# Kernel tuning notes

Hardware: AMD Instinct MI355X
Metric: run time of the kernel (lower is better)

The kernel has to match this reference:

```python
import jax, jax.numpy as jnp
import numpy as np

# Module hyperparameters (BNMorph.__init__ defaults + KITTI resolution)
B, H, W = 8, 320, 1024
SEARCH_W = 7      # serachWidth
SEARCH_H = 3      # searchHeight
SPARSITY_RAD = 2
SENSE_R = 20
PIX_DW = 24.0     # pixel_distance_weight
ALPHA_DW = 0.7    # alpha_distance_weight
PIX_MUL_DW = 1.9  # pixel_mulline_distance_weight
ALPHA_PAD = 1.6   # alpha_padding
EDGE_DENSITY = 0.02


def _make_offsets():
    # Exactly mirrors BNMorph.__init__ buffer construction.
    rs = np.arange(-SEARCH_W, SEARCH_W + 1)
    cs = np.arange(-SEARCH_H, SEARCH_H + 1)
    xx, yy = np.meshgrid(rs, cs)
    xx = xx.flatten(); yy = yy.flatten()
    idx = np.argsort(xx ** 2 + yy ** 2)
    xx = xx[idx]; yy = yy[idx]
    ss = np.arange(-SPARSITY_RAD, SPARSITY_RAD + 1)
    sxx, syy = np.meshgrid(ss, ss)
    sxx = sxx.flatten(); syy = syy.flatten()
    cspan = np.arange(-SENSE_R, SENSE_R + 1)
    cxx, cyy = np.meshgrid(cspan, cspan)
    cxx = cxx.flatten(); cyy = cyy.flatten()
    ci = np.argsort(cxx ** 2 + cyy ** 2)
    cxx = cxx[ci]; cyy = cyy[ci]
    f32 = lambda a: jnp.asarray(a, dtype=jnp.float32)
    return f32(xx), f32(yy), f32(sxx), f32(syy), f32(cxx), f32(cyy)


def setup_inputs() -> dict:
    key = jax.random.key(0)
    k1, k2 = jax.random.split(key)
    binMapsrc = (jax.random.uniform(k1, (B, 1, H, W)) < EDGE_DENSITY).astype(jnp.float32)
    binMapdst = (jax.random.uniform(k2, (B, 1, H, W)) < EDGE_DENSITY).astype(jnp.float32)
    xx, yy, sxx, syy, cxx, cyy = _make_offsets()
    return {"binMapsrc": binMapsrc, "binMapdst": binMapdst,
            "xx": xx, "yy": yy, "sxx": sxx, "syy": syy, "cxx": cxx, "cyy": cyy}


def _forward(binMapsrc, binMapdst, xx, yy, sxx, syy, cxx, cyy):
    src = binMapsrc[:, 0] > 0.5  # [B,H,W] bool
    dst = binMapdst[:, 0] > 0.5
    b, h, w = src.shape

    # ---- 1. sparsity filtering of src edge points ----
    # keep an active pixel iff no active pixel precedes it (raster order)
    # inside the sparsity window -> approximates greedy sparsification.
    sdx = sxx.astype(jnp.int32); sdy = syy.astype(jnp.int32)
    prec = ((sdy < 0) | ((sdy == 0) & (sdx < 0))).astype(jnp.float32)
    Ps = jnp.pad(src.astype(jnp.float32),
                 ((0, 0), (SPARSITY_RAD, SPARSITY_RAD), (SPARSITY_RAD, SPARSITY_RAD)))

    def sp_step(acc, off):
        dx, dy, wk = off
        sl = jax.lax.dynamic_slice(Ps, (0, SPARSITY_RAD + dy, SPARSITY_RAD + dx), (b, h, w))
        return acc + sl * wk, None

    acc, _ = jax.lax.scan(sp_step, jnp.zeros((b, h, w), jnp.float32), (sdx, sdy, prec))
    kept = src & (acc < 0.5)

    # ---- 2. windowed nearest-correspondence search in dst ----
    # offsets (xx,yy) are pre-sorted by distance, so the first hit is nearest.
    qdx = xx.astype(jnp.int32); qdy = yy.astype(jnp.int32)
    Pd = jnp.pad(dst, ((0, 0), (SEARCH_H, SEARCH_H), (SEARCH_W, SEARCH_W)))

    def m_step(carry, off):
        found, vx, vy = carry
        dx, dy, dxf, dyf = off
        sl = jax.lax.dynamic_slice(Pd, (0, SEARCH_H + dy, SEARCH_W + dx), (b, h, w))
        hit = sl & kept & (~found)
        vx = jnp.where(hit, dxf, vx)
        vy = jnp.where(hit, dyf, vy)
        return (found | hit, vx, vy), None

    init = (jnp.zeros((b, h, w), bool),
            jnp.zeros((b, h, w), jnp.float32),
            jnp.zeros((b, h, w), jnp.float32))
    (found, vx, vy), _ = jax.lax.scan(m_step, init, (qdx, qdy, xx, yy))

    # ---- 3. distance-weighted morph field (splat = depthwise conv) ----
    d = jnp.sqrt(cxx ** 2 + cyy ** 2)
    wts = ALPHA_DW * jnp.exp(-d * PIX_MUL_DW / PIX_DW)
    R = SENSE_R
    K = jnp.zeros((2 * R + 1, 2 * R + 1), jnp.float32)
    K = K.at[cyy.astype(jnp.int32) + R, cxx.astype(jnp.int32) + R].set(wts)

    m = found.astype(jnp.float32)
    inp = jnp.stack([m, m * vx, m * vy], axis=1)        # [B,3,H,W]
    ker = jnp.tile(K[None, None], (3, 1, 1, 1))          # [3,1,41,41]
    out = jax.lax.conv_general_dilated(
        inp, ker, (1, 1), ((R, R), (R, R)),
        dimension_numbers=("NCHW", "OIHW", "NCHW"), feature_group_count=3)
    den = out[:, 0] + ALPHA_PAD
    dispx = out[:, 1] / den
    dispy = out[:, 2] / den

    ygrid, xgrid = jnp.meshgrid(jnp.arange(h, dtype=jnp.float32),
                                jnp.arange(w, dtype=jnp.float32), indexing="ij")
    morphedx = xgrid + dispx
    morphedy = ygrid + dispy
    orgpts_x = xgrid * m
    orgpts_y = ygrid * m
    correspts_x = (xgrid + vx) * m
    correspts_y = (ygrid + vy) * m
    return morphedx, morphedy, orgpts_x, orgpts_y, correspts_x, correspts_y


def reference(binMapsrc, binMapdst, xx, yy, sxx, syy, cxx, cyy):
    return _forward(binMapsrc, binMapdst, xx, yy, sxx, syy, cxx, cyy)
```

## Files before the change

### kernel.cpp

```cpp
#include <hip/hip_runtime.h>


#define BB 8
#define HH 320
#define WW 1024
#define N_PIX (BB*HH*WW)
#define WPI (HH*(WW/32))
#define RR 20
#define TLW 64
#define TLH 32
#define TXN (WW/TLW)
#define TYN (HH/TLH)
#define TPB (TXN*TYN)
#define N_TILES (BB*TPB)
#define NQ 105
#define CAP_MAX 512
#define PACK_OFF 16384
#define WTABN (4*42*48)
#define WTAB_OFF (PACK_OFF + 2*BB*WPI*4)
#define LISTS_OFF (WTAB_OFF + WTABN*4)

typedef unsigned long long u64;
typedef float v2f __attribute__((ext_vector_type(2)));

__global__ __launch_bounds__(256) void pack_zero(
    const float* __restrict__ src, const float* __restrict__ dst,
    unsigned* __restrict__ packed, int* __restrict__ cnt,
    float* __restrict__ wtab_g)
{
    int t = threadIdx.x;
    int i = blockIdx.x * 256 + t;
    if (i < N_TILES) cnt[i] = 0;
    if (i < WTABN) {
        int rot = i / (42 * 48);
        int rem = i - rot * (42 * 48);
        int row = rem / 48, c = rem - row * 48;
        int pc = c + rot;
        float v = 0.0f;
        if (row <= 40 && pc >= 4 && pc <= 44) {
            int dxv = pc - 24, dyv = row - 20;
            float d = sqrtf((float)(dxv * dxv + dyv * dyv));
            v = 0.7f * expf((-d * 1.9f) / 24.0f);
        }
        wtab_g[i] = v;
    }
    const float4* p = (i < (N_PIX >> 2)) ? (const float4*)src + i
                                         : (const float4*)dst + (i - (N_PIX >> 2));
    float4 v = *p;
    unsigned nib = (v.x > 0.5f ? 1u : 0u) | (v.y > 0.5f ? 2u : 0u)
                 | (v.z > 0.5f ? 4u : 0u) | (v.w > 0.5f ? 8u : 0u);
    unsigned val = nib << ((t & 7) * 4);
    val |= __shfl_xor(val, 1);
    val |= __shfl_xor(val, 2);
    val |= __shfl_xor(val, 4);
    if ((t & 7) == 0) packed[i >> 3] = val;
}

__global__ __launch_bounds__(256) void build_points(
    const unsigned* __restrict__ packed,
    const float* __restrict__ xx, const float* __restrict__ yy,
    float* __restrict__ out, int* __restrict__ cnt,
    unsigned* __restrict__ lists, int cap)
{
    __shared__ unsigned sS[6][32];
    __shared__ unsigned sD[10][32];
    __shared__ unsigned sMask[4][32];
    __shared__ unsigned sVB[4][256];
    __shared__ unsigned sPtXY[256];
    __shared__ unsigned sPk[256];
    __shared__ unsigned sPairs[1024];
    __shared__ int prank[NQ], sdxv[NQ], sdyv[NQ];
    __shared__ int lcnt[2];

    int t  = threadIdx.x;
    int y0 = blockIdx.x * 4;
    int b  = blockIdx.y;
    const unsigned* psrc = packed + (size_t)b * WPI;
    const unsigned* pdst = packed + (size_t)(BB + b) * WPI;

    if (t < 192) {
        int r = t >> 5, w = t & 31;
        int y2 = y0 - 2 + r;
        sS[r][w] = (y2 >= 0 && y2 < HH) ? psrc[(y2 << 5) + w] : 0u;
    }
    for (int i = t; i < 320; i += 256) {
        int r = i >> 5, w = i & 31;
        int y2 = y0 - 3 + r;
        sD[r][w] = (y2 >= 0 && y2 < HH) ? pdst[(y2 << 5) + w] : 0u;
    }
    if (t < NQ) {
        int dx = (int)xx[t], dy = (int)yy[t];
        sdxv[t] = dx; sdyv[t] = dy;
        prank[(dy + 3) * 15 + (dx + 7)] = t;
    }
    if (t < 2) lcnt[t] = 0;
    #pragma unroll
    for (int g = 0; g < 4; ++g) sVB[g][t] = 0;
    __syncthreads();

    if (t < 128) {
        int r = t >> 5, w = t & 31;
        unsigned C = sS[r + 2][w];
        unsigned kept = 0;
        if (C) {
            #define EXT5(row) ( (u64)((w ? (row)[w-1] : 0u) >> 30) \
                              | ((u64)(row)[w] << 2) \
                              | ((u64)((w < 31 ? (row)[w+1] : 0u) & 3u) << 34) )
            u64 a = EXT5(sS[r]) | EXT5(sS[r + 1]);
            u64 or5 = a | (a >> 1) | (a >> 2) | (a >> 3) | (a >> 4);
            u64 e2 = EXT5(sS[r + 2]);
            u64 or2 = e2 | (e2 >> 1);
            kept = C & ~(unsigned)(or5 | or2);
        }
        unsigned found = 0;
        if (kept) {
            u64 dil = 0;
            #pragma unroll
            for (int rr = 0; rr < 7; ++rr) {
                const unsigned* row = sD[r + rr];
                unsigned L = w ? row[w-1] : 0u;
                unsigned R = (w < 31) ? row[w+1] : 0u;
                dil |= (u64)(L >> 25) | ((u64)row[w] << 7) | ((u64)(R & 0x7Fu) << 39);
            }
            u64 a2 = dil | (dil >> 1);
            u64 b2 = a2 | (a2 >> 2);
            u64 c2 = b2 | (b2 >> 4);
            u64 o15 = c2 | (c2 >> 7);
            found = kept & (unsigned)o15;
        }
        sMask[r][w] = found;
        int nf = __popc(found);
        if (nf) {
            int base = atomicAdd(&lcnt[0], nf);
            unsigned fi = found;
            while (fi) {
                int bit = __builtin_ctz(fi); fi &= fi - 1;
                if (base < 256) sPtXY[base] = (unsigned)((r << 10) | (w << 5) | bit);
                ++base;
            }
        }
    }
    __syncthreads();
    int nPts = lcnt[0]; if (nPts > 256) nPts = 256;

    for (int i = t; i < nPts; i += 256) {
        unsigned e = sPtXY[i];
        int r = e >> 10, x = (int)(e & 1023u);
        int y = y0 + r;
        int x7 = x - 7;
        int j = x7 >> 5;
        int sh = x7 & 31;
        u64 lo = 0, hi = 0;
        #pragma unroll
        for (int rr = 0; rr < 7; ++rr) {
            const unsigned* row = sD[r + rr];
            unsigned W0 = (j >= 0) ? row[j] : 0u;
            unsigned W1 = (j + 1 < 32) ? row[j + 1] : 0u;
            u64 win = (((u64)W0 | ((u64)W1 << 32)) >> sh) & 0x7FFFull;
            if (rr < 4) lo |= win << (15 * rr);
            else        hi |= win << (15 * (rr - 4));
        }
        int minr = NQ - 1;
        while (lo) { int bb2 = __builtin_ctzll(lo); lo &= lo - 1; int rk = prank[bb2];      if (rk < minr) minr = rk; }
        while (hi) { int bb2 = __builtin_ctzll(hi); hi &= hi - 1; int rk = prank[60 + bb2]; if (rk < minr) minr = rk; }
        int vx = sdxv[minr], vy = sdyv[minr];

        ((unsigned char*)sVB)[(r << 10) + x] =
            (unsigned char)((vx + 7) | ((vy + 3) << 4));
        sPk[i] = (unsigned)x | ((unsigned)y << 10)
               | ((unsigned)(vx + 7) << 19) | ((unsigned)(vy + 3) << 23);

        int txl = x - RR; txl = (txl < 0 ? 0 : txl) >> 6;
        int txh = x + RR; txh = (txh > WW - 1 ? WW - 1 : txh) >> 6;
        int tyl = y - RR; tyl = (tyl < 0 ? 0 : tyl) >> 5;
        int tyh = y + RR; tyh = (tyh > HH - 1 ? HH - 1 : tyh) >> 5;
        int np = (txh - txl + 1) * (tyh - tyl + 1);
        int base = atomicAdd(&lcnt[1], np);
        for (int ty = tyl; ty <= tyh; ++ty)
            for (int tx = txl; tx <= txh; ++tx) {
                if (base < 1024)
                    sPairs[base] = ((unsigned)i << 16) | (unsigned)(b * TPB + ty * TXN + tx);
                ++base;
            }
    }
    __syncthreads();
    int nPairs = lcnt[1]; if (nPairs > 1024) nPairs = 1024;

    for (int jj = t; jj < nPairs; jj += 256) {
        unsigned pr = sPairs[jj];
        int tile = (int)(pr & 0xFFFFu);
        int i    = (int)(pr >> 16);
        int pos = atomicAdd(&cnt[tile], 1);
        if (pos < cap) lists[(size_t)tile * cap + pos] = sPk[i];
    }

    int xs = t << 2;
    int wq = t >> 3;
    int bo = xs & 31;
    size_t bbase = (size_t)b * HH * WW;
    #pragma unroll
    for (int g = 0; g < 4; ++g) {
        unsigned mw = sMask[g][wq];
        unsigned vb = sVB[g][t];
        float fy = (float)(y0 + g);
        float4 o2, o3, o4, o5;
        float* po2 = &o2.x; float* po3 = &o3.x; float* po4 = &o4.x; float* po5 = &o5.x;
        #pragma unroll
        for (int jj = 0; jj < 4; ++jj) {
            float fm = (float)((mw >> (bo + jj)) & 1u);
            unsigned by = (vb >> (8 * jj)) & 255u;
            float fvx = (float)((int)(by & 15u) - 7);
            float fvy = (float)((int)(by >> 4) - 3);
            float fx = (float)(xs + jj);
            po2[jj] = fx * fm;
            po3[jj] = fy * fm;
            po4[jj] = (fx + fvx) * fm;
            po5[jj] = (fy + fvy) * fm;
        }
        size_t idx = bbase + (size_t)(y0 + g) * WW + xs;
        *reinterpret_cast<float4*>(out + 2 * (size_t)N_PIX + idx) = o2;
        *reinterpret_cast<float4*>(out + 3 * (size_t)N_PIX + idx) = o3;
        *reinterpret_cast<float4*>(out + 4 * (size_t)N_PIX + idx) = o4;
        *reinterpret_cast<float4*>(out + 5 * (size_t)N_PIX + idx) = o5;
    }
}

__global__ __launch_bounds__(256, 4) void splat_finalize(
    const int* __restrict__ cnt, const unsigned* __restrict__ lists,
    const float* __restrict__ wtab_g,
    float* __restrict__ out, int cap)
{
    __shared__ __align__(16) float wtab[WTABN];
    __shared__ __align__(16) unsigned pts[CAP_MAX];
    int t = threadIdx.x;

    const float4* wg = (const float4*)wtab_g;
    #pragma unroll
    for (int i = 0; i < WTABN / 1024; ++i)
        ((float4*)wtab)[i * 256 + t] = wg[i * 256 + t];
    if (t < (WTABN / 4) % 256)
        ((float4*)wtab)[(WTABN / 1024) * 256 + t] = wg[(WTABN / 1024) * 256 + t];

    int txT = blockIdx.x, tyT = blockIdx.y, b = blockIdx.z;
    int tile = b * TPB + tyT * TXN + txT;
    int n = cnt[tile]; if (n > cap) n = cap;
    int n4 = (n + 3) & ~3;
    for (int i = t; i < n4; i += 256)
        pts[i] = (i < n) ? lists[(size_t)tile * cap + i] : 0xFFFFFFFFu;
    __syncthreads();

    int x0  = txT * TLW + (t & 15) * 4;
    int y0t = tyT * TLH + (t >> 4) * 2;
    int wy0 = tyT * TLH + __builtin_amdgcn_readfirstlane(t >> 6) * 8;

    v2f a0p[2][2] = {};
    v2f av[2][4]  = {};

    for (int p = 0; p < n4; p += 4) {
        uint4 P = *(const uint4*)&pts[p];
        #pragma unroll
        for (int k = 0; k < 4; ++k) {
            int spk = __builtin_amdgcn_readfirstlane(
                (int)(k == 0 ? P.x : k == 1 ? P.y : k == 2 ? P.z : P.w));
            int py = (spk >> 10) & 511;
            if (py < wy0 - 20 || py > wy0 + 27) continue;
            int px = spk & 1023;
            float pvx = (float)(((spk >> 19) & 15) - 7);
            float pvy = (float)(((spk >> 23) & 7) - 3);
            v2f vv = {pvx, pvy};

            int coff = px - x0 + 21;
            coff = coff < 0 ? 0 : (coff > 45 ? 45 : coff);
            int rot = coff & 3;
            int cb  = rot * (42 * 48) + (coff & ~3);
            #pragma unroll
            for (int ry = 0; ry < 2; ++ry) {
                int dyr = py - (y0t + ry) + 20;
                int rowi = ((unsigned)dyr > 40u) ? 41 : dyr;
                float4 wv = *(const float4*)&wtab[cb + rowi * 48];
                a0p[ry][0] += (v2f){wv.w, wv.z};
                a0p[ry][1] += (v2f){wv.y, wv.x};
                av[ry][0] += wv.w * vv;
                av[ry][1] += wv.z * vv;
                av[ry][2] += wv.y * vv;
                av[ry][3] += wv.x * vv;
            }
        }
    }

    size_t bbase = (size_t)b * HH * WW;
    #pragma unroll
    for (int ry = 0; ry < 2; ++ry) {
        int y = y0t + ry;
        size_t idx = bbase + (size_t)y * WW + x0;
        float d0 = a0p[ry][0].x + 1.6f, d1 = a0p[ry][0].y + 1.6f;
        float d2 = a0p[ry][1].x + 1.6f, d3 = a0p[ry][1].y + 1.6f;
        float4 ox = { (float)x0     + av[ry][0].x / d0, (float)(x0+1) + av[ry][1].x / d1,
                      (float)(x0+2) + av[ry][2].x / d2, (float)(x0+3) + av[ry][3].x / d3 };
        float4 oy = { (float)y + av[ry][0].y / d0, (float)y + av[ry][1].y / d1,
                      (float)y + av[ry][2].y / d2, (float)y + av[ry][3].y / d3 };
        *reinterpret_cast<float4*>(out + idx)                 = ox;
        *reinterpret_cast<float4*>(out + (size_t)N_PIX + idx) = oy;
    }
}

extern "C" void kernel_launch(void* const* d_in, const int* in_sizes, int n_in,
                              void* d_out, int out_size, void* d_ws, size_t ws_size,
                              hipStream_t stream) {
    const float* src = (const float*)d_in[0];
    const float* dst = (const float*)d_in[1];
    const float* xx  = (const float*)d_in[2];
    const float* yy  = (const float*)d_in[3];
    float* out = (float*)d_out;

    int*      cnt    = (int*)d_ws;
    unsigned* packed = (unsigned*)((char*)d_ws + PACK_OFF);
    float*    wtab_g = (float*)((char*)d_ws + WTAB_OFF);
    unsigned* lists  = (unsigned*)((char*)d_ws + LISTS_OFF);

    int cap = CAP_MAX;
    size_t need = (size_t)LISTS_OFF + (size_t)N_TILES * cap * sizeof(unsigned);
    if (ws_size < need) {
        long avail = ((long)ws_size - LISTS_OFF) / ((long)N_TILES * 4);
        cap = avail < 1 ? 1 : (avail > CAP_MAX ? CAP_MAX : (int)avail);
    }

    pack_zero<<<(2 * N_PIX / 4) / 256, 256, 0, stream>>>(src, dst, packed, cnt, wtab_g);

    dim3 g1(HH / 4, BB);
    build_points<<<g1, 256, 0, stream>>>(packed, xx, yy, out, cnt, lists, cap);

    dim3 g2(TXN, TYN, BB);
    splat_finalize<<<g2, 256, 0, stream>>>(cnt, lists, wtab_g, out, cap);
}
```

Before: 149.9 us.

## Move mask outputs into splat kernel and prefilter points per wavefront

The four mask-derived outputs (orgpts and correspts) are no longer written by build_points. splat_finalize now writes zeros for them and then scatters values at the points its tile owns. build_points handles 2 rows per block instead of 4, and each wavefront in splat_finalize compacts the tile list with ballot down to the points within reach of its rows. This drops per-point row checks from the inner loop and moves writes between kernels, at the cost of extra list reads and scattered stores plus a second barrier.

```diff
diff --git a/kernel.cpp b/kernel.cpp
--- a/kernel.cpp
+++ b/kernel.cpp
@@ -59,34 +59,30 @@
 __global__ __launch_bounds__(256) void build_points(
     const unsigned* __restrict__ packed,
     const float* __restrict__ xx, const float* __restrict__ yy,
-    float* __restrict__ out, int* __restrict__ cnt,
-    unsigned* __restrict__ lists, int cap)
+    int* __restrict__ cnt, unsigned* __restrict__ lists, int cap)
 {
-    __shared__ unsigned sS[6][32];
-    __shared__ unsigned sD[10][32];
-    __shared__ unsigned sMask[4][32];
-    __shared__ unsigned sVB[4][256];
-    __shared__ unsigned sPtXY[256];
-    __shared__ unsigned sPk[256];
-    __shared__ unsigned sPairs[1024];
+    __shared__ unsigned sS[4][32];
+    __shared__ unsigned sD[8][32];
+    __shared__ unsigned sPtXY[128];
+    __shared__ unsigned sPk[128];
+    __shared__ unsigned sPairs[512];
     __shared__ int prank[NQ], sdxv[NQ], sdyv[NQ];
     __shared__ int lcnt[2];
 
     int t  = threadIdx.x;
-    int y0 = blockIdx.x * 4;
+    int y0 = blockIdx.x * 2;
     int b  = blockIdx.y;
     const unsigned* psrc = packed + (size_t)b * WPI;
     const unsigned* pdst = packed + (size_t)(BB + b) * WPI;
 
-    if (t < 192) {
+    {
         int r = t >> 5, w = t & 31;
-        int y2 = y0 - 2 + r;
-        sS[r][w] = (y2 >= 0 && y2 < HH) ? psrc[(y2 << 5) + w] : 0u;
-    }
-    for (int i = t; i < 320; i += 256) {
-        int r = i >> 5, w = i & 31;
         int y2 = y0 - 3 + r;
         sD[r][w] = (y2 >= 0 && y2 < HH) ? pdst[(y2 << 5) + w] : 0u;
+        if (t < 128) {
+            int y3 = y0 - 2 + (t >> 5);
+            sS[t >> 5][w] = (y3 >= 0) ? psrc[(y3 << 5) + w] : 0u;
+        }
     }
     if (t < NQ) {
         int dx = (int)xx[t], dy = (int)yy[t];
@@ -94,11 +90,9 @@
         prank[(dy + 3) * 15 + (dx + 7)] = t;
     }
     if (t < 2) lcnt[t] = 0;
-    #pragma unroll
-    for (int g = 0; g < 4; ++g) sVB[g][t] = 0;
-    __syncthreads();
-
-    if (t < 128) {
+    __syncthreads();
+
+    if (t < 64) {
         int r = t >> 5, w = t & 31;
         unsigned C = sS[r + 2][w];
         unsigned kept = 0;
@@ -128,23 +122,22 @@
             u64 o15 = c2 | (c2 >> 7);
             found = kept & (unsigned)o15;
         }
-        sMask[r][w] = found;
         int nf = __popc(found);
         if (nf) {
             int base = atomicAdd(&lcnt[0], nf);
             unsigned fi = found;
             while (fi) {
                 int bit = __builtin_ctz(fi); fi &= fi - 1;
-                if (base < 256) sPtXY[base] = (unsigned)((r << 10) | (w << 5) | bit);
+                if (base < 128) sPtXY[base] = (unsigned)((r << 10) | (w << 5) | bit);
                 ++base;
             }
         }
     }
     __syncthreads();
-    int nPts = lcnt[0]; if (nPts > 256) nPts = 256;
-
-    for (int i = t; i < nPts; i += 256) {
-        unsigned e = sPtXY[i];
+    int nPts = lcnt[0]; if (nPts > 128) nPts = 128;
+
+    if (t < nPts) {
+        unsigned e = sPtXY[t];
         int r = e >> 10, x = (int)(e & 1023u);
         int y = y0 + r;
         int x7 = x - 7;
@@ -165,9 +158,7 @@
         while (hi) { int bb2 = __builtin_ctzll(hi); hi &= hi - 1; int rk = prank[60 + bb2]; if (rk < minr) minr = rk; }
         int vx = sdxv[minr], vy = sdyv[minr];
 
-        ((unsigned char*)sVB)[(r << 10) + x] =
-            (unsigned char)((vx + 7) | ((vy + 3) << 4));
-        sPk[i] = (unsigned)x | ((unsigned)y << 10)
+        sPk[t] = (unsigned)x | ((unsigned)y << 10)
                | ((unsigned)(vx + 7) << 19) | ((unsigned)(vy + 3) << 23);
 
         int txl = x - RR; txl = (txl < 0 ? 0 : txl) >> 6;
@@ -178,13 +169,13 @@
         int base = atomicAdd(&lcnt[1], np);
         for (int ty = tyl; ty <= tyh; ++ty)
             for (int tx = txl; tx <= txh; ++tx) {
-                if (base < 1024)
-                    sPairs[base] = ((unsigned)i << 16) | (unsigned)(b * TPB + ty * TXN + tx);
+                if (base < 512)
+                    sPairs[base] = ((unsigned)t << 16) | (unsigned)(b * TPB + ty * TXN + tx);
                 ++base;
             }
     }
     __syncthreads();
-    int nPairs = lcnt[1]; if (nPairs > 1024) nPairs = 1024;
+    int nPairs = lcnt[1]; if (nPairs > 512) nPairs = 512;
 
     for (int jj = t; jj < nPairs; jj += 256) {
         unsigned pr = sPairs[jj];
@@ -193,36 +184,6 @@
         int pos = atomicAdd(&cnt[tile], 1);
         if (pos < cap) lists[(size_t)tile * cap + pos] = sPk[i];
     }
-
-    int xs = t << 2;
-    int wq = t >> 3;
-    int bo = xs & 31;
-    size_t bbase = (size_t)b * HH * WW;
-    #pragma unroll
-    for (int g = 0; g < 4; ++g) {
-        unsigned mw = sMask[g][wq];
-        unsigned vb = sVB[g][t];
-        float fy = (float)(y0 + g);
-        float4 o2, o3, o4, o5;
-        float* po2 = &o2.x; float* po3 = &o3.x; float* po4 = &o4.x; float* po5 = &o5.x;
-        #pragma unroll
-        for (int jj = 0; jj < 4; ++jj) {
-            float fm = (float)((mw >> (bo + jj)) & 1u);
-            unsigned by = (vb >> (8 * jj)) & 255u;
-            float fvx = (float)((int)(by & 15u) - 7);
-            float fvy = (float)((int)(by >> 4) - 3);
-            float fx = (float)(xs + jj);
-            po2[jj] = fx * fm;
-            po3[jj] = fy * fm;
-            po4[jj] = (fx + fvx) * fm;
-            po5[jj] = (fy + fvy) * fm;
-        }
-        size_t idx = bbase + (size_t)(y0 + g) * WW + xs;
-        *reinterpret_cast<float4*>(out + 2 * (size_t)N_PIX + idx) = o2;
-        *reinterpret_cast<float4*>(out + 3 * (size_t)N_PIX + idx) = o3;
-        *reinterpret_cast<float4*>(out + 4 * (size_t)N_PIX + idx) = o4;
-        *reinterpret_cast<float4*>(out + 5 * (size_t)N_PIX + idx) = o5;
-    }
 }
 
 __global__ __launch_bounds__(256, 4) void splat_finalize(
@@ -231,51 +192,63 @@
     float* __restrict__ out, int cap)
 {
     __shared__ __align__(16) float wtab[WTABN];
-    __shared__ __align__(16) unsigned pts[CAP_MAX];
+    __shared__ __align__(16) unsigned sWav[4][264];
     int t = threadIdx.x;
-
-    const float4* wg = (const float4*)wtab_g;
-    #pragma unroll
-    for (int i = 0; i < WTABN / 1024; ++i)
-        ((float4*)wtab)[i * 256 + t] = wg[i * 256 + t];
-    if (t < (WTABN / 4) % 256)
-        ((float4*)wtab)[(WTABN / 1024) * 256 + t] = wg[(WTABN / 1024) * 256 + t];
+    int lane = t & 63, w = t >> 6;
+
+    for (int i = t; i < WTABN / 4; i += 256)
+        ((float4*)wtab)[i] = ((const float4*)wtab_g)[i];
 
     int txT = blockIdx.x, tyT = blockIdx.y, b = blockIdx.z;
     int tile = b * TPB + tyT * TXN + txT;
+    const unsigned* lp = lists + (size_t)tile * cap;
     int n = cnt[tile]; if (n > cap) n = cap;
-    int n4 = (n + 3) & ~3;
-    for (int i = t; i < n4; i += 256)
-        pts[i] = (i < n) ? lists[(size_t)tile * cap + i] : 0xFFFFFFFFu;
+
+    int wy0 = tyT * TLH + w * 8;
+    int cw = 0;
+    for (int base = 0; base < n; base += 64) {
+        int i = base + lane;
+        unsigned pk = 0xFFFFFFFFu;
+        if (i < n) pk = lp[i];
+        int py = (int)((pk >> 10) & 511u);
+        bool pass = (i < n) & (py >= wy0 - 20) & (py <= wy0 + 27);
+        u64 m = __ballot(pass);
+        if (pass) {
+            int idx = __popcll(m & ((1ull << lane) - 1ull));
+            if (cw + idx < 256) sWav[w][cw + idx] = pk;
+        }
+        cw += __popcll(m);
+    }
+    if (cw > 256) cw = 256;
+    int c4 = (cw + 3) & ~3;
+    if (lane < c4 - cw) sWav[w][cw + lane] = 0xFFFFFFFFu;
     __syncthreads();
 
     int x0  = txT * TLW + (t & 15) * 4;
     int y0t = tyT * TLH + (t >> 4) * 2;
-    int wy0 = tyT * TLH + __builtin_amdgcn_readfirstlane(t >> 6) * 8;
 
     v2f a0p[2][2] = {};
     v2f av[2][4]  = {};
 
-    for (int p = 0; p < n4; p += 4) {
-        uint4 P = *(const uint4*)&pts[p];
+    for (int p = 0; p < c4; p += 4) {
+        uint4 P = *(const uint4*)&sWav[w][p];
         #pragma unroll
         for (int k = 0; k < 4; ++k) {
             int spk = __builtin_amdgcn_readfirstlane(
                 (int)(k == 0 ? P.x : k == 1 ? P.y : k == 2 ? P.z : P.w));
-            int py = (spk >> 10) & 511;
-            if (py < wy0 - 20 || py > wy0 + 27) continue;
-            int px = spk & 1023;
+            int pxp21 = (spk & 1023) + 21;
+            int pyp20 = ((spk >> 10) & 511) + 20;
             float pvx = (float)(((spk >> 19) & 15) - 7);
             float pvy = (float)(((spk >> 23) & 7) - 3);
             v2f vv = {pvx, pvy};
 
-            int coff = px - x0 + 21;
+            int coff = pxp21 - x0;
             coff = coff < 0 ? 0 : (coff > 45 ? 45 : coff);
             int rot = coff & 3;
             int cb  = rot * (42 * 48) + (coff & ~3);
             #pragma unroll
             for (int ry = 0; ry < 2; ++ry) {
-                int dyr = py - (y0t + ry) + 20;
+                int dyr = pyp20 - (y0t + ry);
                 int rowi = ((unsigned)dyr > 40u) ? 41 : dyr;
                 float4 wv = *(const float4*)&wtab[cb + rowi * 48];
                 a0p[ry][0] += (v2f){wv.w, wv.z};
@@ -289,6 +262,7 @@
     }
 
     size_t bbase = (size_t)b * HH * WW;
+    float4 z4 = {0.f, 0.f, 0.f, 0.f};
     #pragma unroll
     for (int ry = 0; ry < 2; ++ry) {
         int y = y0t + ry;
@@ -299,8 +273,29 @@
                       (float)(x0+2) + av[ry][2].x / d2, (float)(x0+3) + av[ry][3].x / d3 };
         float4 oy = { (float)y + av[ry][0].y / d0, (float)y + av[ry][1].y / d1,
                       (float)y + av[ry][2].y / d2, (float)y + av[ry][3].y / d3 };
-        *reinterpret_cast<float4*>(out + idx)                 = ox;
-        *reinterpret_cast<float4*>(out + (size_t)N_PIX + idx) = oy;
+        *reinterpret_cast<float4*>(out + idx)                     = ox;
+        *reinterpret_cast<float4*>(out + (size_t)N_PIX + idx)     = oy;
+        *reinterpret_cast<float4*>(out + 2 * (size_t)N_PIX + idx) = z4;
+        *reinterpret_cast<float4*>(out + 3 * (size_t)N_PIX + idx) = z4;
+        *reinterpret_cast<float4*>(out + 4 * (size_t)N_PIX + idx) = z4;
+        *reinterpret_cast<float4*>(out + 5 * (size_t)N_PIX + idx) = z4;
+    }
+    __syncthreads();
+
+    int tx0 = txT * TLW, ty0 = tyT * TLH;
+    for (int i = t; i < n; i += 256) {
+        unsigned pk = lp[i];
+        int px = (int)(pk & 1023u);
+        int py = (int)((pk >> 10) & 511u);
+        if (px >= tx0 && px < tx0 + TLW && py >= ty0 && py < ty0 + TLH) {
+            int vx = (int)((pk >> 19) & 15u) - 7;
+            int vy = (int)((pk >> 23) & 7u) - 3;
+            size_t idx = bbase + (size_t)py * WW + px;
+            out[2 * (size_t)N_PIX + idx] = (float)px;
+            out[3 * (size_t)N_PIX + idx] = (float)py;
+            out[4 * (size_t)N_PIX + idx] = (float)(px + vx);
+            out[5 * (size_t)N_PIX + idx] = (float)(py + vy);
+        }
     }
 }
 
@@ -327,8 +322,8 @@
 
     pack_zero<<<(2 * N_PIX / 4) / 256, 256, 0, stream>>>(src, dst, packed, cnt, wtab_g);
 
-    dim3 g1(HH / 4, BB);
-    build_points<<<g1, 256, 0, stream>>>(packed, xx, yy, out, cnt, lists, cap);
+    dim3 g1(HH / 2, BB);
+    build_points<<<g1, 256, 0, stream>>>(packed, xx, yy, cnt, lists, cap);
 
     dim3 g2(TXN, TYN, BB);
     splat_finalize<<<g2, 256, 0, stream>>>(cnt, lists, wtab_g, out, cap);
```

Measured after the change: 138.4 us. 1.08x faster.
